# Kernel tuning notes

Measured on AMD Instinct MI355X. Metric: run time of the kernel, lower is better.

## Reference

```python
import jax, jax.numpy as jnp
import numpy as np

NEG_POS_RATIO = 3
B, N, C = 32, 32768, 21


def setup_inputs() -> dict:
    key = jax.random.key(0)
    k1, k2, k3, k4, k5 = jax.random.split(key, 5)
    confidence = jax.random.normal(k1, (B, N, C), dtype=jnp.float32)
    predicted_locations = jax.random.normal(k2, (B, N, 5), dtype=jnp.float32)
    gt_locations = jax.random.normal(k3, (B, N, 5), dtype=jnp.float32)
    raw = jax.random.randint(k4, (B, N), 1, C)
    is_pos = jax.random.uniform(k5, (B, N)) < 0.03
    labels = jnp.where(is_pos, raw, 0).astype(jnp.int32)
    return {
        "confidence": confidence,
        "predicted_locations": predicted_locations,
        "labels": labels,
        "gt_locations": gt_locations,
    }


def reference(confidence, predicted_locations, labels, gt_locations):
    # log-softmax over classes once; reused for mining and CE
    logp = jax.nn.log_softmax(confidence, axis=2)          # [B, N, C]

    # --- hard negative mining (no-grad in original) ---
    mining_loss = -jax.lax.stop_gradient(logp[:, :, 0])    # [B, N]
    pos_mask = labels > 0                                   # [B, N]
    num_pos = jnp.sum(pos_mask, axis=1, keepdims=True)      # [B, 1]
    num_neg = num_pos * NEG_POS_RATIO
    loss_m = jnp.where(pos_mask, -jnp.inf, mining_loss)
    idx = jnp.argsort(-loss_m, axis=1)      # descending sort indices
    orders = jnp.argsort(idx, axis=1)       # rank of each prior
    neg_mask = orders < num_neg
    mask = pos_mask | neg_mask

    # --- classification: summed CE over selected priors ---
    ce = -jnp.take_along_axis(logp, labels[..., None].astype(jnp.int32), axis=2)[..., 0]
    classification_loss = jnp.sum(jnp.where(mask, ce, 0.0))

    # --- localization: summed SmoothL1 over positive priors ---
    d = jnp.abs(predicted_locations - gt_locations)
    sl1 = jnp.where(d < 1.0, 0.5 * d * d, d - 0.5)
    smooth_l1_loss = jnp.sum(jnp.where(pos_mask[..., None], sl1, 0.0))

    n_pos = jnp.sum(pos_mask).astype(confidence.dtype)
    return (smooth_l1_loss / n_pos, classification_loss / n_pos)
```

## Files before the change

kernel.cpp:

```cpp
#include <hip/hip_runtime.h>
#include <cstdint>

#define BB 32
#define NN 32768
#define CC 21
#define K1_BLK 256
#define PPT 2
#define TILE (K1_BLK * PPT)
#define K1_GRID ((BB * NN) / TILE)
#define BLKROW (NN / TILE)

#define K2T 1024
#define KPT (NN / K2T)
#define NC 16

typedef float f4 __attribute__((ext_vector_type(4)));

__device__ __forceinline__ float fexp2(float x) {
    float r; asm("v_exp_f32 %0, %1" : "=v"(r) : "v"(x)); return r;
}
__device__ __forceinline__ float flog2(float x) {
    float r; asm("v_log_f32 %0, %1" : "=v"(r) : "v"(x)); return r;
}

__global__ __launch_bounds__(K1_BLK) void k1_compute(
    const float* __restrict__ conf, const float* __restrict__ pred,
    const int* __restrict__ labels, const float* __restrict__ gt,
    unsigned* __restrict__ keys, float* __restrict__ pce,
    float* __restrict__ psl1, int* __restrict__ pcnt)
{
    __shared__ float wce[4], wsl[4];
    __shared__ int   wcnt[4];

    const int tid = threadIdx.x;
    const int lane = tid & 63;
    const int wid = tid >> 6;
    const size_t p0 = (size_t)blockIdx.x * TILE + tid;
    const size_t p1 = p0 + K1_BLK;

    const int lab0 = labels[p0];
    const int lab1 = labels[p1];
    const float* cp0 = conf + p0 * CC;
    const float* cp1 = conf + p1 * CC;
    f4 A0, A1, A2, A3, A4, B0, B1, B2, B3, B4;
    __builtin_memcpy(&A0, cp0 +  0, 16);
    __builtin_memcpy(&A1, cp0 +  4, 16);
    __builtin_memcpy(&A2, cp0 +  8, 16);
    __builtin_memcpy(&A3, cp0 + 12, 16);
    __builtin_memcpy(&A4, cp0 + 16, 16);
    __builtin_memcpy(&B0, cp1 +  0, 16);
    __builtin_memcpy(&B1, cp1 +  4, 16);
    __builtin_memcpy(&B2, cp1 +  8, 16);
    __builtin_memcpy(&B3, cp1 + 12, 16);
    __builtin_memcpy(&B4, cp1 + 16, 16);
    const float a20 = cp0[20];
    const float b20 = cp1[20];

    const bool pos0 = lab0 > 0;
    const bool pos1 = lab1 > 0;

    float sl = 0.f;
    if (pos0) {
        const float* pp = pred + p0 * 5;
        const float* gg = gt + p0 * 5;
#pragma unroll
        for (int j = 0; j < 5; ++j) {
            float d = fabsf(pp[j] - gg[j]);
            sl += (d < 1.f) ? 0.5f * d * d : (d - 0.5f);
        }
    }
    if (pos1) {
        const float* pp = pred + p1 * 5;
        const float* gg = gt + p1 * 5;
#pragma unroll
        for (int j = 0; j < 5; ++j) {
            float d = fabsf(pp[j] - gg[j]);
            sl += (d < 1.f) ? 0.5f * d * d : (d - 0.5f);
        }
    }

    float s0 = 0.f, cl0 = 0.f;
#define KS(Q, J, IDX, LAB, SACC, CACC) { const float v_ = Q[J]; \
        SACC += fexp2(v_ * 1.44269504f); \
        CACC = ((IDX) == (LAB)) ? v_ : CACC; }
    KS(A0,0,0,lab0,s0,cl0) KS(A0,1,1,lab0,s0,cl0) KS(A0,2,2,lab0,s0,cl0) KS(A0,3,3,lab0,s0,cl0)
    KS(A1,0,4,lab0,s0,cl0) KS(A1,1,5,lab0,s0,cl0) KS(A1,2,6,lab0,s0,cl0) KS(A1,3,7,lab0,s0,cl0)
    KS(A2,0,8,lab0,s0,cl0) KS(A2,1,9,lab0,s0,cl0) KS(A2,2,10,lab0,s0,cl0) KS(A2,3,11,lab0,s0,cl0)
    KS(A3,0,12,lab0,s0,cl0) KS(A3,1,13,lab0,s0,cl0) KS(A3,2,14,lab0,s0,cl0) KS(A3,3,15,lab0,s0,cl0)
    KS(A4,0,16,lab0,s0,cl0) KS(A4,1,17,lab0,s0,cl0) KS(A4,2,18,lab0,s0,cl0) KS(A4,3,19,lab0,s0,cl0)
    { const float v_ = a20; s0 += fexp2(v_ * 1.44269504f); cl0 = (20 == lab0) ? v_ : cl0; }
    const float lse0 = 0.6931471805599453f * flog2(s0);
    const float mining0 = fmaxf(lse0 - A0[0], 0.f);
    keys[p0] = pos0 ? 0u : __float_as_uint(mining0);
    float ce = pos0 ? (lse0 - cl0) : 0.f;
    int cnt = pos0 ? 1 : 0;

    float s1 = 0.f, cl1 = 0.f;
    KS(B0,0,0,lab1,s1,cl1) KS(B0,1,1,lab1,s1,cl1) KS(B0,2,2,lab1,s1,cl1) KS(B0,3,3,lab1,s1,cl1)
    KS(B1,0,4,lab1,s1,cl1) KS(B1,1,5,lab1,s1,cl1) KS(B1,2,6,lab1,s1,cl1) KS(B1,3,7,lab1,s1,cl1)
    KS(B2,0,8,lab1,s1,cl1) KS(B2,1,9,lab1,s1,cl1) KS(B2,2,10,lab1,s1,cl1) KS(B2,3,11,lab1,s1,cl1)
    KS(B3,0,12,lab1,s1,cl1) KS(B3,1,13,lab1,s1,cl1) KS(B3,2,14,lab1,s1,cl1) KS(B3,3,15,lab1,s1,cl1)
    KS(B4,0,16,lab1,s1,cl1) KS(B4,1,17,lab1,s1,cl1) KS(B4,2,18,lab1,s1,cl1) KS(B4,3,19,lab1,s1,cl1)
    { const float v_ = b20; s1 += fexp2(v_ * 1.44269504f); cl1 = (20 == lab1) ? v_ : cl1; }
#undef KS
    const float lse1 = 0.6931471805599453f * flog2(s1);
    const float mining1 = fmaxf(lse1 - B0[0], 0.f);
    keys[p1] = pos1 ? 0u : __float_as_uint(mining1);
    ce += pos1 ? (lse1 - cl1) : 0.f;
    cnt += pos1 ? 1 : 0;

#pragma unroll
    for (int d = 32; d > 0; d >>= 1) {
        ce  += __shfl_down(ce, d);
        sl  += __shfl_down(sl, d);
        cnt += __shfl_down(cnt, d);
    }
    if (lane == 0) { wce[wid] = ce; wsl[wid] = sl; wcnt[wid] = cnt; }
    __syncthreads();
    if (tid == 0) {
        float tce = 0.f, tsl = 0.f; int tc = 0;
#pragma unroll
        for (int w = 0; w < 4; ++w) { tce += wce[w]; tsl += wsl[w]; tc += wcnt[w]; }
        pce[blockIdx.x]  = tce;
        psl1[blockIdx.x] = tsl;
        pcnt[blockIdx.x] = tc;
    }
}

template <class GET>
__device__ __forceinline__ void sscan2048(
    GET get, unsigned* ss, unsigned* swsum,
    int* s_bin, int* s_above, unsigned want, int tid, int lane, int wid)
{
    const int b0 = 2047 - 2 * tid;
    const int b1 = 2046 - 2 * tid;
    const unsigned m0 = get(b0), m1 = get(b1);
    unsigned v = m0 + m1;
#pragma unroll
    for (int d = 1; d < 64; d <<= 1) {
        unsigned u = __shfl_up(v, d);
        if (lane >= d) v += u;
    }
    if (lane == 63) swsum[wid] = v;
    __syncthreads();
    if (wid == 0) {
        unsigned wv = (lane < 16) ? swsum[lane] : 0;
#pragma unroll
        for (int d = 1; d < 16; d <<= 1) {
            unsigned u = __shfl_up(wv, d);
            if (lane >= d) wv += u;
        }
        if (lane < 16) swsum[lane] = wv;
    }
    __syncthreads();
    const unsigned off = wid ? swsum[wid - 1] : 0;
    const unsigned incl = off + v;
    const unsigned sb0 = incl - m1;
    ss[b0] = sb0;
    ss[b1] = incl;
    __syncthreads();
    if (sb0 >= want && (b0 == 2047 || ss[b0 + 1] < want)) {
        *s_bin = b0; *s_above = (b0 == 2047) ? 0 : (int)ss[b0 + 1];
    }
    if (incl >= want && ss[b1 + 1] < want) {
        *s_bin = b1; *s_above = (int)ss[b1 + 1];
    }
    __syncthreads();
}

__global__ __launch_bounds__(K2T) void k2_select(
    const unsigned* __restrict__ keys, const int* __restrict__ pcnt,
    double* __restrict__ row_sumneg)
{
    const int b = blockIdx.x;
    const int tid = threadIdx.x;
    const int lane = tid & 63;
    const int wid = tid >> 6;
    const unsigned* rk = keys + (size_t)b * NN;

    __shared__ unsigned h1[1024 * NC];
    __shared__ unsigned ss[2048];
    __shared__ unsigned swsum[16];
    __shared__ double sdred[16];
    __shared__ int s_bin, s_above;
    __shared__ unsigned s_want;

    uint4 kv[8];
    const uint4* rk4 = reinterpret_cast<const uint4*>(rk);
#pragma unroll
    for (int j = 0; j < 8; ++j) kv[j] = rk4[tid + j * K2T];

    if (wid == 0) {
        int c = pcnt[b * BLKROW + lane];
#pragma unroll
        for (int d = 32; d > 0; d >>= 1) c += __shfl_down(c, d);
        if (lane == 0) s_want = (unsigned)((3 * c > NN) ? NN : 3 * c);
    }
    for (int i = tid; i < 1024 * NC; i += K2T) h1[i] = 0;
    __syncthreads();
    const unsigned want = s_want;
    if (want == 0) { if (tid == 0) row_sumneg[b] = 0.0; return; }

    const unsigned cp = lane & (NC - 1);
#pragma unroll
    for (int j = 0; j < 8; ++j) {
        atomicAdd(&h1[((kv[j].x >> 21) << 4) | cp], 1u);
        atomicAdd(&h1[((kv[j].y >> 21) << 4) | cp], 1u);
        atomicAdd(&h1[((kv[j].z >> 21) << 4) | cp], 1u);
        atomicAdd(&h1[((kv[j].w >> 21) << 4) | cp], 1u);
    }
    __syncthreads();

    {
        const int bn = 1023 - tid;
        unsigned mv = 0;
#pragma unroll
        for (int c = 0; c < NC; ++c) mv += h1[(bn << 4) | c];
        unsigned v = mv;
#pragma unroll
        for (int d = 1; d < 64; d <<= 1) {
            unsigned u = __shfl_up(v, d);
            if (lane >= d) v += u;
        }
        if (lane == 63) swsum[wid] = v;
        __syncthreads();
        if (wid == 0) {
            unsigned wv = (lane < 16) ? swsum[lane] : 0;
#pragma unroll
            for (int d = 1; d < 16; d <<= 1) {
                unsigned u = __shfl_up(wv, d);
                if (lane >= d) wv += u;
            }
            if (lane < 16) swsum[lane] = wv;
        }
        __syncthreads();
        const unsigned incl = (wid ? swsum[wid - 1] : 0) + v;
        ss[bn] = incl;
        __syncthreads();
        if (incl >= want && (bn == 1023 || ss[bn + 1] < want)) {
            s_bin = bn; s_above = (bn == 1023) ? 0 : (int)ss[bn + 1];
        }
        __syncthreads();
    }
    const unsigned bsel1 = (unsigned)s_bin;
    const unsigned want1 = want - (unsigned)s_above;

    for (int i = tid; i < 4096; i += K2T) h1[i] = 0;
    __syncthreads();
    const unsigned c2 = lane & 1;
#pragma unroll
    for (int j = 0; j < 8; ++j) {
#define L2ADD(K) if (((K) >> 21) == bsel1) \
        atomicAdd(&h1[((((K) >> 10) & 0x7FFu) << 1) | c2], 1u);
        L2ADD(kv[j].x) L2ADD(kv[j].y) L2ADD(kv[j].z) L2ADD(kv[j].w)
#undef L2ADD
    }
    __syncthreads();
    sscan2048([&](int bn) { return h1[bn << 1] + h1[(bn << 1) | 1]; },
              ss, swsum, &s_bin, &s_above, want1, tid, lane, wid);
    const unsigned bsel2 = (unsigned)s_bin;
    const unsigned want2 = want1 - (unsigned)s_above;

    for (int i = tid; i < 4096; i += K2T) h1[i] = 0;
    __syncthreads();
    const unsigned pref = (bsel1 << 11) | bsel2;
#pragma unroll
    for (int j = 0; j < 8; ++j) {
#define L3ADD(K) if (((K) >> 10) == pref) \
        atomicAdd(&h1[(((K) & 0x3FFu) << 1) | c2], 1u);
        L3ADD(kv[j].x) L3ADD(kv[j].y) L3ADD(kv[j].z) L3ADD(kv[j].w)
#undef L3ADD
    }
    __syncthreads();
    sscan2048([&](int bn) { return h1[bn << 1] + h1[(bn << 1) | 1]; },
              ss, swsum, &s_bin, &s_above, want2, tid, lane, wid);
    const unsigned T = (bsel1 << 21) | (bsel2 << 10) | (unsigned)s_bin;

    int above = 0;
    double sel = 0.0;
#pragma unroll
    for (int j = 0; j < 8; ++j) {
#define FIN(K) if ((K) > T) { above++; sel += (double)__uint_as_float(K); }
        FIN(kv[j].x) FIN(kv[j].y) FIN(kv[j].z) FIN(kv[j].w)
#undef FIN
    }
#pragma unroll
    for (int d = 32; d > 0; d >>= 1) {
        above += __shfl_down(above, d);
        sel   += __shfl_down(sel, d);
    }
    if (lane == 0) { swsum[wid] = (unsigned)above; sdred[wid] = sel; }
    __syncthreads();
    if (tid == 0) {
        unsigned atot = 0; double stot = 0.0;
#pragma unroll
        for (int w = 0; w < 16; ++w) { atot += swsum[w]; stot += sdred[w]; }
        const int r = (int)want - (int)atot;
        row_sumneg[b] = stot + (double)r * (double)__uint_as_float(T);
    }
}

__global__ __launch_bounds__(256) void k3_final(
    const float* __restrict__ pce, const float* __restrict__ psl1,
    const int* __restrict__ pcnt, const double* __restrict__ row_sumneg,
    float* __restrict__ out)
{
    __shared__ double a[256], c[256];
    __shared__ int ic[256];
    const int tid = threadIdx.x;
    double ce = 0.0, sl = 0.0; int np = 0;
    for (int i = tid; i < K1_GRID; i += 256) {
        ce += (double)pce[i];
        sl += (double)psl1[i];
        np += pcnt[i];
    }
    a[tid] = ce; c[tid] = sl; ic[tid] = np;
    __syncthreads();
    for (int st = 128; st > 0; st >>= 1) {
        if (tid < st) {
            a[tid] += a[tid + st];
            c[tid] += c[tid + st];
            ic[tid] += ic[tid + st];
        }
        __syncthreads();
    }
    if (tid == 0) {
        double ns = 0.0;
        for (int bb = 0; bb < BB; ++bb) ns += row_sumneg[bb];
        const double npos = (double)ic[0];
        out[0] = (float)(c[0] / npos);
        out[1] = (float)((a[0] + ns) / npos);
    }
}

extern "C" void kernel_launch(void* const* d_in, const int* in_sizes, int n_in,
                              void* d_out, int out_size, void* d_ws, size_t ws_size,
                              hipStream_t stream)
{
    const float* conf   = (const float*)d_in[0];
    const float* pred   = (const float*)d_in[1];
    const int*   labels = (const int*)d_in[2];
    const float* gt     = (const float*)d_in[3];
    float* out = (float*)d_out;

    char* ws = (char*)d_ws;
    unsigned* keys       = (unsigned*)ws;
    float*    pce        = (float*)(ws + 4194304);
    float*    psl1       = (float*)(ws + 4202496);
    int*      pcnt       = (int*)(ws + 4210688);
    double*   row_sumneg = (double*)(ws + 4218880);

    k1_compute<<<K1_GRID, K1_BLK, 0, stream>>>(conf, pred, labels, gt,
                                               keys, pce, psl1, pcnt);
    k2_select<<<BB, K2T, 0, stream>>>(keys, pcnt, row_sumneg);
    k3_final<<<1, 256, 0, stream>>>(pce, psl1, pcnt, row_sumneg, out);
}
```

Baseline: 39.52 us.

## Build per-block top-level histograms in k1 and fold final reduction into k2

k1 now builds a 2048-bin (top 11 bits) histogram of mining keys for each 512-prior tile in shared memory and writes it out as packed 16-bit counts. k2 then sums these 64 partial histograms per row instead of running the first-level shared-memory atomic pass over all 32K keys. The separate k3 reduction kernel is removed: the last k2 block to finish, detected with an atomic counter and threadfence, computes the final outputs. This saves one launch and the heaviest atomic pass, at the cost of extra LDS atomics and a 4 MB histogram write in k1, plus strided 16-bit reads in k2.

```diff
diff --git a/kernel.cpp b/kernel.cpp
--- a/kernel.cpp
+++ b/kernel.cpp
@@ -11,8 +11,6 @@
 #define BLKROW (NN / TILE)
 
 #define K2T 1024
-#define KPT (NN / K2T)
-#define NC 16
 
 typedef float f4 __attribute__((ext_vector_type(4)));
 
@@ -27,8 +25,10 @@
     const float* __restrict__ conf, const float* __restrict__ pred,
     const int* __restrict__ labels, const float* __restrict__ gt,
     unsigned* __restrict__ keys, float* __restrict__ pce,
-    float* __restrict__ psl1, int* __restrict__ pcnt)
+    float* __restrict__ psl1, int* __restrict__ pcnt,
+    unsigned short* __restrict__ bhist, unsigned* __restrict__ done)
 {
+    __shared__ unsigned h4[4096];
     __shared__ float wce[4], wsl[4];
     __shared__ int   wcnt[4];
 
@@ -37,6 +37,11 @@
     const int wid = tid >> 6;
     const size_t p0 = (size_t)blockIdx.x * TILE + tid;
     const size_t p1 = p0 + K1_BLK;
+
+    if (blockIdx.x == 0 && tid == 0) *done = 0u;
+
+#pragma unroll
+    for (int i = 0; i < 16; ++i) h4[tid + i * K1_BLK] = 0;
 
     const int lab0 = labels[p0];
     const int lab1 = labels[p1];
@@ -91,7 +96,8 @@
     { const float v_ = a20; s0 += fexp2(v_ * 1.44269504f); cl0 = (20 == lab0) ? v_ : cl0; }
     const float lse0 = 0.6931471805599453f * flog2(s0);
     const float mining0 = fmaxf(lse0 - A0[0], 0.f);
-    keys[p0] = pos0 ? 0u : __float_as_uint(mining0);
+    const unsigned key0 = pos0 ? 0u : __float_as_uint(mining0);
+    keys[p0] = key0;
     float ce = pos0 ? (lse0 - cl0) : 0.f;
     int cnt = pos0 ? 1 : 0;
 
@@ -105,7 +111,8 @@
 #undef KS
     const float lse1 = 0.6931471805599453f * flog2(s1);
     const float mining1 = fmaxf(lse1 - B0[0], 0.f);
-    keys[p1] = pos1 ? 0u : __float_as_uint(mining1);
+    const unsigned key1 = pos1 ? 0u : __float_as_uint(mining1);
+    keys[p1] = key1;
     ce += pos1 ? (lse1 - cl1) : 0.f;
     cnt += pos1 ? 1 : 0;
 
@@ -117,6 +124,11 @@
     }
     if (lane == 0) { wce[wid] = ce; wsl[wid] = sl; wcnt[wid] = cnt; }
     __syncthreads();
+
+    const unsigned c4i = lane & 3;
+    atomicAdd(&h4[((key0 >> 21) << 2) | c4i], 1u);
+    atomicAdd(&h4[((key1 >> 21) << 2) | c4i], 1u);
+
     if (tid == 0) {
         float tce = 0.f, tsl = 0.f; int tc = 0;
 #pragma unroll
@@ -125,6 +137,17 @@
         psl1[blockIdx.x] = tsl;
         pcnt[blockIdx.x] = tc;
     }
+    __syncthreads();
+
+    const int b0 = tid << 2;
+    const unsigned n0 = h4[(b0 << 2)] + h4[(b0 << 2) | 1] + h4[(b0 << 2) | 2] + h4[(b0 << 2) | 3];
+    const unsigned n1 = h4[((b0 + 1) << 2)] + h4[((b0 + 1) << 2) | 1] + h4[((b0 + 1) << 2) | 2] + h4[((b0 + 1) << 2) | 3];
+    const unsigned n2 = h4[((b0 + 2) << 2)] + h4[((b0 + 2) << 2) | 1] + h4[((b0 + 2) << 2) | 2] + h4[((b0 + 2) << 2) | 3];
+    const unsigned n3 = h4[((b0 + 3) << 2)] + h4[((b0 + 3) << 2) | 1] + h4[((b0 + 3) << 2) | 2] + h4[((b0 + 3) << 2) | 3];
+    uint2 pk;
+    pk.x = n0 | (n1 << 16);
+    pk.y = n2 | (n3 << 16);
+    reinterpret_cast<uint2*>(bhist + (size_t)blockIdx.x * 1024)[tid] = pk;
 }
 
 template <class GET>
@@ -170,7 +193,10 @@
 
 __global__ __launch_bounds__(K2T) void k2_select(
     const unsigned* __restrict__ keys, const int* __restrict__ pcnt,
-    double* __restrict__ row_sumneg)
+    const unsigned short* __restrict__ bhist,
+    const float* __restrict__ pce, const float* __restrict__ psl1,
+    double* __restrict__ row_sumneg, unsigned* __restrict__ done,
+    float* __restrict__ out)
 {
     const int b = blockIdx.x;
     const int tid = threadIdx.x;
@@ -178,11 +204,13 @@
     const int wid = tid >> 6;
     const unsigned* rk = keys + (size_t)b * NN;
 
-    __shared__ unsigned h1[1024 * NC];
+    __shared__ unsigned h1[4096];
     __shared__ unsigned ss[2048];
     __shared__ unsigned swsum[16];
     __shared__ double sdred[16];
-    __shared__ int s_bin, s_above;
+    __shared__ double fA[16], fB[16];
+    __shared__ int fI[16];
+    __shared__ int s_bin, s_above, s_last;
     __shared__ unsigned s_want;
 
     uint4 kv[8];
@@ -196,140 +224,132 @@
         for (int d = 32; d > 0; d >>= 1) c += __shfl_down(c, d);
         if (lane == 0) s_want = (unsigned)((3 * c > NN) ? NN : 3 * c);
     }
-    for (int i = tid; i < 1024 * NC; i += K2T) h1[i] = 0;
     __syncthreads();
     const unsigned want = s_want;
-    if (want == 0) { if (tid == 0) row_sumneg[b] = 0.0; return; }
-
-    const unsigned cp = lane & (NC - 1);
-#pragma unroll
-    for (int j = 0; j < 8; ++j) {
-        atomicAdd(&h1[((kv[j].x >> 21) << 4) | cp], 1u);
-        atomicAdd(&h1[((kv[j].y >> 21) << 4) | cp], 1u);
-        atomicAdd(&h1[((kv[j].z >> 21) << 4) | cp], 1u);
-        atomicAdd(&h1[((kv[j].w >> 21) << 4) | cp], 1u);
-    }
-    __syncthreads();
-
-    {
+
+    if (want > 0) {
         const int bn = 1023 - tid;
+        const unsigned short* bh = bhist + (size_t)b * BLKROW * 1024;
         unsigned mv = 0;
-#pragma unroll
-        for (int c = 0; c < NC; ++c) mv += h1[(bn << 4) | c];
-        unsigned v = mv;
-#pragma unroll
-        for (int d = 1; d < 64; d <<= 1) {
-            unsigned u = __shfl_up(v, d);
-            if (lane >= d) v += u;
-        }
-        if (lane == 63) swsum[wid] = v;
-        __syncthreads();
-        if (wid == 0) {
-            unsigned wv = (lane < 16) ? swsum[lane] : 0;
-#pragma unroll
-            for (int d = 1; d < 16; d <<= 1) {
-                unsigned u = __shfl_up(wv, d);
-                if (lane >= d) wv += u;
+#pragma unroll 8
+        for (int j = 0; j < BLKROW; ++j) mv += bh[j * 1024 + bn];
+
+        {
+            unsigned v = mv;
+#pragma unroll
+            for (int d = 1; d < 64; d <<= 1) {
+                unsigned u = __shfl_up(v, d);
+                if (lane >= d) v += u;
             }
-            if (lane < 16) swsum[lane] = wv;
-        }
-        __syncthreads();
-        const unsigned incl = (wid ? swsum[wid - 1] : 0) + v;
-        ss[bn] = incl;
-        __syncthreads();
-        if (incl >= want && (bn == 1023 || ss[bn + 1] < want)) {
-            s_bin = bn; s_above = (bn == 1023) ? 0 : (int)ss[bn + 1];
-        }
-        __syncthreads();
-    }
-    const unsigned bsel1 = (unsigned)s_bin;
-    const unsigned want1 = want - (unsigned)s_above;
-
-    for (int i = tid; i < 4096; i += K2T) h1[i] = 0;
-    __syncthreads();
-    const unsigned c2 = lane & 1;
-#pragma unroll
-    for (int j = 0; j < 8; ++j) {
+            if (lane == 63) swsum[wid] = v;
+            __syncthreads();
+            if (wid == 0) {
+                unsigned wv = (lane < 16) ? swsum[lane] : 0;
+#pragma unroll
+                for (int d = 1; d < 16; d <<= 1) {
+                    unsigned u = __shfl_up(wv, d);
+                    if (lane >= d) wv += u;
+                }
+                if (lane < 16) swsum[lane] = wv;
+            }
+            __syncthreads();
+            const unsigned incl = (wid ? swsum[wid - 1] : 0) + v;
+            ss[bn] = incl;
+            __syncthreads();
+            if (incl >= want && (bn == 1023 || ss[bn + 1] < want)) {
+                s_bin = bn; s_above = (bn == 1023) ? 0 : (int)ss[bn + 1];
+            }
+            __syncthreads();
+        }
+        const unsigned bsel1 = (unsigned)s_bin;
+        const unsigned want1 = want - (unsigned)s_above;
+
+        for (int i = tid; i < 4096; i += K2T) h1[i] = 0;
+        __syncthreads();
+        const unsigned c2 = lane & 1;
+#pragma unroll
+        for (int j = 0; j < 8; ++j) {
 #define L2ADD(K) if (((K) >> 21) == bsel1) \
-        atomicAdd(&h1[((((K) >> 10) & 0x7FFu) << 1) | c2], 1u);
-        L2ADD(kv[j].x) L2ADD(kv[j].y) L2ADD(kv[j].z) L2ADD(kv[j].w)
+            atomicAdd(&h1[((((K) >> 10) & 0x7FFu) << 1) | c2], 1u);
+            L2ADD(kv[j].x) L2ADD(kv[j].y) L2ADD(kv[j].z) L2ADD(kv[j].w)
 #undef L2ADD
-    }
-    __syncthreads();
-    sscan2048([&](int bn) { return h1[bn << 1] + h1[(bn << 1) | 1]; },
-              ss, swsum, &s_bin, &s_above, want1, tid, lane, wid);
-    const unsigned bsel2 = (unsigned)s_bin;
-    const unsigned want2 = want1 - (unsigned)s_above;
-
-    for (int i = tid; i < 4096; i += K2T) h1[i] = 0;
-    __syncthreads();
-    const unsigned pref = (bsel1 << 11) | bsel2;
-#pragma unroll
-    for (int j = 0; j < 8; ++j) {
+        }
+        __syncthreads();
+        sscan2048([&](int bb2) { return h1[bb2 << 1] + h1[(bb2 << 1) | 1]; },
+                  ss, swsum, &s_bin, &s_above, want1, tid, lane, wid);
+        const unsigned bsel2 = (unsigned)s_bin;
+        const unsigned want2 = want1 - (unsigned)s_above;
+
+        for (int i = tid; i < 4096; i += K2T) h1[i] = 0;
+        __syncthreads();
+        const unsigned pref = (bsel1 << 11) | bsel2;
+#pragma unroll
+        for (int j = 0; j < 8; ++j) {
 #define L3ADD(K) if (((K) >> 10) == pref) \
-        atomicAdd(&h1[(((K) & 0x3FFu) << 1) | c2], 1u);
-        L3ADD(kv[j].x) L3ADD(kv[j].y) L3ADD(kv[j].z) L3ADD(kv[j].w)
+            atomicAdd(&h1[(((K) & 0x3FFu) << 1) | c2], 1u);
+            L3ADD(kv[j].x) L3ADD(kv[j].y) L3ADD(kv[j].z) L3ADD(kv[j].w)
 #undef L3ADD
-    }
-    __syncthreads();
-    sscan2048([&](int bn) { return h1[bn << 1] + h1[(bn << 1) | 1]; },
-              ss, swsum, &s_bin, &s_above, want2, tid, lane, wid);
-    const unsigned T = (bsel1 << 21) | (bsel2 << 10) | (unsigned)s_bin;
-
-    int above = 0;
-    double sel = 0.0;
-#pragma unroll
-    for (int j = 0; j < 8; ++j) {
+        }
+        __syncthreads();
+        sscan2048([&](int bb2) { return h1[bb2 << 1] + h1[(bb2 << 1) | 1]; },
+                  ss, swsum, &s_bin, &s_above, want2, tid, lane, wid);
+        const unsigned T = (bsel1 << 21) | (bsel2 << 10) | (unsigned)s_bin;
+
+        int above = 0;
+        double sel = 0.0;
+#pragma unroll
+        for (int j = 0; j < 8; ++j) {
 #define FIN(K) if ((K) > T) { above++; sel += (double)__uint_as_float(K); }
-        FIN(kv[j].x) FIN(kv[j].y) FIN(kv[j].z) FIN(kv[j].w)
+            FIN(kv[j].x) FIN(kv[j].y) FIN(kv[j].z) FIN(kv[j].w)
 #undef FIN
-    }
-#pragma unroll
-    for (int d = 32; d > 0; d >>= 1) {
-        above += __shfl_down(above, d);
-        sel   += __shfl_down(sel, d);
-    }
-    if (lane == 0) { swsum[wid] = (unsigned)above; sdred[wid] = sel; }
-    __syncthreads();
-    if (tid == 0) {
-        unsigned atot = 0; double stot = 0.0;
-#pragma unroll
-        for (int w = 0; w < 16; ++w) { atot += swsum[w]; stot += sdred[w]; }
-        const int r = (int)want - (int)atot;
-        row_sumneg[b] = stot + (double)r * (double)__uint_as_float(T);
-    }
-}
-
-__global__ __launch_bounds__(256) void k3_final(
-    const float* __restrict__ pce, const float* __restrict__ psl1,
-    const int* __restrict__ pcnt, const double* __restrict__ row_sumneg,
-    float* __restrict__ out)
-{
-    __shared__ double a[256], c[256];
-    __shared__ int ic[256];
-    const int tid = threadIdx.x;
-    double ce = 0.0, sl = 0.0; int np = 0;
-    for (int i = tid; i < K1_GRID; i += 256) {
-        ce += (double)pce[i];
-        sl += (double)psl1[i];
-        np += pcnt[i];
-    }
-    a[tid] = ce; c[tid] = sl; ic[tid] = np;
-    __syncthreads();
-    for (int st = 128; st > 0; st >>= 1) {
-        if (tid < st) {
-            a[tid] += a[tid + st];
-            c[tid] += c[tid + st];
-            ic[tid] += ic[tid + st];
-        }
-        __syncthreads();
-    }
-    if (tid == 0) {
-        double ns = 0.0;
-        for (int bb = 0; bb < BB; ++bb) ns += row_sumneg[bb];
-        const double npos = (double)ic[0];
-        out[0] = (float)(c[0] / npos);
-        out[1] = (float)((a[0] + ns) / npos);
+        }
+#pragma unroll
+        for (int d = 32; d > 0; d >>= 1) {
+            above += __shfl_down(above, d);
+            sel   += __shfl_down(sel, d);
+        }
+        if (lane == 0) { swsum[wid] = (unsigned)above; sdred[wid] = sel; }
+        __syncthreads();
+        if (tid == 0) {
+            unsigned atot = 0; double stot = 0.0;
+#pragma unroll
+            for (int w = 0; w < 16; ++w) { atot += swsum[w]; stot += sdred[w]; }
+            const int r = (int)want - (int)atot;
+            row_sumneg[b] = stot + (double)r * (double)__uint_as_float(T);
+        }
+    } else {
+        if (tid == 0) row_sumneg[b] = 0.0;
+    }
+
+    __threadfence();
+    if (tid == 0) s_last = (atomicAdd(done, 1u) == BB - 1) ? 1 : 0;
+    __syncthreads();
+    if (s_last) {
+        __threadfence();
+        double ce = 0.0, sl = 0.0; int np = 0;
+        for (int i = tid; i < K1_GRID; i += K2T) {
+            ce += (double)pce[i];
+            sl += (double)psl1[i];
+            np += pcnt[i];
+        }
+#pragma unroll
+        for (int d = 32; d > 0; d >>= 1) {
+            ce += __shfl_down(ce, d);
+            sl += __shfl_down(sl, d);
+            np += __shfl_down(np, d);
+        }
+        if (lane == 0) { fA[wid] = ce; fB[wid] = sl; fI[wid] = np; }
+        __syncthreads();
+        if (tid == 0) {
+            double tce = 0.0, tsl = 0.0; int tnp = 0;
+#pragma unroll
+            for (int w = 0; w < 16; ++w) { tce += fA[w]; tsl += fB[w]; tnp += fI[w]; }
+            double ns = 0.0;
+            for (int bb = 0; bb < BB; ++bb) ns += row_sumneg[bb];
+            const double npos = (double)tnp;
+            out[0] = (float)(tsl / npos);
+            out[1] = (float)((tce + ns) / npos);
+        }
     }
 }
 
@@ -344,14 +364,17 @@
     float* out = (float*)d_out;
 
     char* ws = (char*)d_ws;
-    unsigned* keys       = (unsigned*)ws;
-    float*    pce        = (float*)(ws + 4194304);
-    float*    psl1       = (float*)(ws + 4202496);
-    int*      pcnt       = (int*)(ws + 4210688);
-    double*   row_sumneg = (double*)(ws + 4218880);
+    unsigned*       keys       = (unsigned*)ws;
+    unsigned short* bhist      = (unsigned short*)(ws + 4194304);
+    float*          pce        = (float*)(ws + 8388608);
+    float*          psl1       = (float*)(ws + 8396800);
+    int*            pcnt       = (int*)(ws + 8404992);
+    double*         row_sumneg = (double*)(ws + 8413184);
+    unsigned*       done       = (unsigned*)(ws + 8413440);
 
     k1_compute<<<K1_GRID, K1_BLK, 0, stream>>>(conf, pred, labels, gt,
-                                               keys, pce, psl1, pcnt);
-    k2_select<<<BB, K2T, 0, stream>>>(keys, pcnt, row_sumneg);
-    k3_final<<<1, 256, 0, stream>>>(pce, psl1, pcnt, row_sumneg, out);
-}
+                                               keys, pce, psl1, pcnt,
+                                               bhist, done);
+    k2_select<<<BB, K2T, 0, stream>>>(keys, pcnt, bhist, pce, psl1,
+                                      row_sumneg, done, out);
+}
```

New measurement: 49.53 us. +25.3%, slower.

## Stage confidence rows into LDS via global_load_lds with one prior per thread

Applied to the files above, without the earlier changes.

Each wave copies its 64 priors' contiguous confidence rows into shared memory using direct global-to-LDS 16-byte loads, so the global reads are fully coalesced instead of strided per-thread vector loads. Each thread now handles one prior instead of two, doubling the grid and the number of per-block partials. The workspace offsets and the per-row count reduction in the selection kernel are updated to match. The cost is LDS traffic with bank conflicts from the 21-float row stride, and less work per thread.

```diff
diff --git a/kernel.cpp b/kernel.cpp
--- a/kernel.cpp
+++ b/kernel.cpp
@@ -5,16 +5,12 @@
 #define NN 32768
 #define CC 21
 #define K1_BLK 256
-#define PPT 2
-#define TILE (K1_BLK * PPT)
-#define K1_GRID ((BB * NN) / TILE)
-#define BLKROW (NN / TILE)
+#define K1_GRID ((BB * NN) / K1_BLK)
+#define BLKROW (NN / K1_BLK)
+#define WSTAGE 1536
 
 #define K2T 1024
-#define KPT (NN / K2T)
 #define NC 16
-
-typedef float f4 __attribute__((ext_vector_type(4)));
 
 __device__ __forceinline__ float fexp2(float x) {
     float r; asm("v_exp_f32 %0, %1" : "=v"(r) : "v"(x)); return r;
@@ -29,85 +25,64 @@
     unsigned* __restrict__ keys, float* __restrict__ pce,
     float* __restrict__ psl1, int* __restrict__ pcnt)
 {
+    __shared__ __align__(16) float lconf[4 * WSTAGE];
     __shared__ float wce[4], wsl[4];
     __shared__ int   wcnt[4];
 
     const int tid = threadIdx.x;
     const int lane = tid & 63;
-    const int wid = tid >> 6;
-    const size_t p0 = (size_t)blockIdx.x * TILE + tid;
-    const size_t p1 = p0 + K1_BLK;
-
-    const int lab0 = labels[p0];
-    const int lab1 = labels[p1];
-    const float* cp0 = conf + p0 * CC;
-    const float* cp1 = conf + p1 * CC;
-    f4 A0, A1, A2, A3, A4, B0, B1, B2, B3, B4;
-    __builtin_memcpy(&A0, cp0 +  0, 16);
-    __builtin_memcpy(&A1, cp0 +  4, 16);
-    __builtin_memcpy(&A2, cp0 +  8, 16);
-    __builtin_memcpy(&A3, cp0 + 12, 16);
-    __builtin_memcpy(&A4, cp0 + 16, 16);
-    __builtin_memcpy(&B0, cp1 +  0, 16);
-    __builtin_memcpy(&B1, cp1 +  4, 16);
-    __builtin_memcpy(&B2, cp1 +  8, 16);
-    __builtin_memcpy(&B3, cp1 + 12, 16);
-    __builtin_memcpy(&B4, cp1 + 16, 16);
-    const float a20 = cp0[20];
-    const float b20 = cp1[20];
-
-    const bool pos0 = lab0 > 0;
-    const bool pos1 = lab1 > 0;
+    const int w = tid >> 6;
+    const size_t p = (size_t)blockIdx.x * K1_BLK + tid;
+
+    const int lab = labels[p];
+
+    const char* gsrc = (const char*)conf +
+        (size_t)(blockIdx.x * K1_BLK + w * 64) * (CC * 4);
+    float* ldst = lconf + w * WSTAGE;
+#pragma unroll
+    for (int s = 0; s < 6; ++s) {
+        int slot = s * 64 + lane;
+        if (s == 5) slot = (slot > 335) ? 335 : slot;
+        __builtin_amdgcn_global_load_lds(
+            (const __attribute__((address_space(1))) unsigned*)
+                (gsrc + (size_t)slot * 16),
+            (__attribute__((address_space(3))) unsigned*)(ldst + s * 256),
+            16, 0, 0);
+    }
+
+    const bool pos = lab > 0;
 
     float sl = 0.f;
-    if (pos0) {
-        const float* pp = pred + p0 * 5;
-        const float* gg = gt + p0 * 5;
+    if (pos) {
+        const float* pp = pred + p * 5;
+        const float* gg = gt + p * 5;
+        float pv[5], gv[5];
+#pragma unroll
+        for (int j = 0; j < 5; ++j) { pv[j] = pp[j]; gv[j] = gg[j]; }
 #pragma unroll
         for (int j = 0; j < 5; ++j) {
-            float d = fabsf(pp[j] - gg[j]);
+            float d = fabsf(pv[j] - gv[j]);
             sl += (d < 1.f) ? 0.5f * d * d : (d - 0.5f);
         }
     }
-    if (pos1) {
-        const float* pp = pred + p1 * 5;
-        const float* gg = gt + p1 * 5;
-#pragma unroll
-        for (int j = 0; j < 5; ++j) {
-            float d = fabsf(pp[j] - gg[j]);
-            sl += (d < 1.f) ? 0.5f * d * d : (d - 0.5f);
-        }
-    }
-
-    float s0 = 0.f, cl0 = 0.f;
-#define KS(Q, J, IDX, LAB, SACC, CACC) { const float v_ = Q[J]; \
-        SACC += fexp2(v_ * 1.44269504f); \
-        CACC = ((IDX) == (LAB)) ? v_ : CACC; }
-    KS(A0,0,0,lab0,s0,cl0) KS(A0,1,1,lab0,s0,cl0) KS(A0,2,2,lab0,s0,cl0) KS(A0,3,3,lab0,s0,cl0)
-    KS(A1,0,4,lab0,s0,cl0) KS(A1,1,5,lab0,s0,cl0) KS(A1,2,6,lab0,s0,cl0) KS(A1,3,7,lab0,s0,cl0)
-    KS(A2,0,8,lab0,s0,cl0) KS(A2,1,9,lab0,s0,cl0) KS(A2,2,10,lab0,s0,cl0) KS(A2,3,11,lab0,s0,cl0)
-    KS(A3,0,12,lab0,s0,cl0) KS(A3,1,13,lab0,s0,cl0) KS(A3,2,14,lab0,s0,cl0) KS(A3,3,15,lab0,s0,cl0)
-    KS(A4,0,16,lab0,s0,cl0) KS(A4,1,17,lab0,s0,cl0) KS(A4,2,18,lab0,s0,cl0) KS(A4,3,19,lab0,s0,cl0)
-    { const float v_ = a20; s0 += fexp2(v_ * 1.44269504f); cl0 = (20 == lab0) ? v_ : cl0; }
-    const float lse0 = 0.6931471805599453f * flog2(s0);
-    const float mining0 = fmaxf(lse0 - A0[0], 0.f);
-    keys[p0] = pos0 ? 0u : __float_as_uint(mining0);
-    float ce = pos0 ? (lse0 - cl0) : 0.f;
-    int cnt = pos0 ? 1 : 0;
-
-    float s1 = 0.f, cl1 = 0.f;
-    KS(B0,0,0,lab1,s1,cl1) KS(B0,1,1,lab1,s1,cl1) KS(B0,2,2,lab1,s1,cl1) KS(B0,3,3,lab1,s1,cl1)
-    KS(B1,0,4,lab1,s1,cl1) KS(B1,1,5,lab1,s1,cl1) KS(B1,2,6,lab1,s1,cl1) KS(B1,3,7,lab1,s1,cl1)
-    KS(B2,0,8,lab1,s1,cl1) KS(B2,1,9,lab1,s1,cl1) KS(B2,2,10,lab1,s1,cl1) KS(B2,3,11,lab1,s1,cl1)
-    KS(B3,0,12,lab1,s1,cl1) KS(B3,1,13,lab1,s1,cl1) KS(B3,2,14,lab1,s1,cl1) KS(B3,3,15,lab1,s1,cl1)
-    KS(B4,0,16,lab1,s1,cl1) KS(B4,1,17,lab1,s1,cl1) KS(B4,2,18,lab1,s1,cl1) KS(B4,3,19,lab1,s1,cl1)
-    { const float v_ = b20; s1 += fexp2(v_ * 1.44269504f); cl1 = (20 == lab1) ? v_ : cl1; }
-#undef KS
-    const float lse1 = 0.6931471805599453f * flog2(s1);
-    const float mining1 = fmaxf(lse1 - B0[0], 0.f);
-    keys[p1] = pos1 ? 0u : __float_as_uint(mining1);
-    ce += pos1 ? (lse1 - cl1) : 0.f;
-    cnt += pos1 ? 1 : 0;
+
+    asm volatile("s_waitcnt vmcnt(0)" ::: "memory");
+    __builtin_amdgcn_sched_barrier(0);
+
+    const float* my = ldst + lane * CC;
+    float s_ = 0.f;
+#pragma unroll
+    for (int c = 0; c < CC; ++c) s_ += fexp2(my[c] * 1.44269504f);
+    const float lse = 0.6931471805599453f * flog2(s_);
+
+    const float c0 = my[0];
+    const float clab = my[lab];
+
+    const float mining = fmaxf(lse - c0, 0.f);
+    keys[p] = pos ? 0u : __float_as_uint(mining);
+
+    float ce = pos ? (lse - clab) : 0.f;
+    int cnt = pos ? 1 : 0;
 
 #pragma unroll
     for (int d = 32; d > 0; d >>= 1) {
@@ -115,12 +90,12 @@
         sl  += __shfl_down(sl, d);
         cnt += __shfl_down(cnt, d);
     }
-    if (lane == 0) { wce[wid] = ce; wsl[wid] = sl; wcnt[wid] = cnt; }
+    if (lane == 0) { wce[w] = ce; wsl[w] = sl; wcnt[w] = cnt; }
     __syncthreads();
     if (tid == 0) {
         float tce = 0.f, tsl = 0.f; int tc = 0;
 #pragma unroll
-        for (int w = 0; w < 4; ++w) { tce += wce[w]; tsl += wsl[w]; tc += wcnt[w]; }
+        for (int v = 0; v < 4; ++v) { tce += wce[v]; tsl += wsl[v]; tc += wcnt[v]; }
         pce[blockIdx.x]  = tce;
         psl1[blockIdx.x] = tsl;
         pcnt[blockIdx.x] = tc;
@@ -191,7 +166,7 @@
     for (int j = 0; j < 8; ++j) kv[j] = rk4[tid + j * K2T];
 
     if (wid == 0) {
-        int c = pcnt[b * BLKROW + lane];
+        int c = pcnt[b * BLKROW + lane] + pcnt[b * BLKROW + 64 + lane];
 #pragma unroll
         for (int d = 32; d > 0; d >>= 1) c += __shfl_down(c, d);
         if (lane == 0) s_want = (unsigned)((3 * c > NN) ? NN : 3 * c);
@@ -346,9 +321,9 @@
     char* ws = (char*)d_ws;
     unsigned* keys       = (unsigned*)ws;
     float*    pce        = (float*)(ws + 4194304);
-    float*    psl1       = (float*)(ws + 4202496);
-    int*      pcnt       = (int*)(ws + 4210688);
-    double*   row_sumneg = (double*)(ws + 4218880);
+    float*    psl1       = (float*)(ws + 4210688);
+    int*      pcnt       = (int*)(ws + 4227072);
+    double*   row_sumneg = (double*)(ws + 4243456);
 
     k1_compute<<<K1_GRID, K1_BLK, 0, stream>>>(conf, pred, labels, gt,
                                                keys, pce, psl1, pcnt);
```

After: 40.78 us. 3.2% more time.
